# Performance work log

Hardware: AMD Instinct MI355X
Metric: run time of the kernel (lower is better)

The kernel has to match this reference:

```python
import jax, jax.numpy as jnp
import numpy as np

VOCAB, EMB, HID = 100000, 300, 600
B, S, N = 256, 64, 64
MAX_LEVEL = 3  # depth of the fixed 4-ary tree


def _tree():
    parent = np.zeros(N, np.int32)
    level = np.zeros(N, np.int32)
    for i in range(1, N):
        parent[i] = (i - 1) // 4
        level[i] = level[parent[i]] + 1
    return parent, level


def setup_inputs() -> dict:
    key = jax.random.key(0)
    ks = jax.random.split(key, 16)
    parent, level = _tree()
    E_tab = jax.random.normal(ks[0], (VOCAB, EMB), jnp.float32) * 0.1
    E_tab = E_tab.at[0].set(0.0)  # padding_idx=0
    return dict(
        premise_x=jax.random.randint(ks[1], (B, S), 0, VOCAB),
        hypothesis_x=jax.random.randint(ks[2], (B, S), 0, VOCAB),
        p_word_idx=jax.random.randint(ks[3], (B, N), -1, S),  # -1 => ones vector
        p_rel_id=jax.random.randint(ks[4], (B, N), -1, 4),    # 0..2 transformed, -1/3 identity
        h_word_idx=jax.random.randint(ks[5], (B, N), -1, S),
        h_rel_id=jax.random.randint(ks[6], (B, N), -1, 4),
        parent=jnp.asarray(parent),
        level=jnp.asarray(level),
        E_tab=E_tab,
        W_enc=jax.random.normal(ks[7], (3, EMB, EMB), jnp.float32) * 0.1,
        W0_w=jax.random.normal(ks[8], (HID, 6 * EMB), jnp.float32) * 0.1,
        W0_b=jax.random.normal(ks[9], (HID,), jnp.float32) * 0.1,
        W1_w=jax.random.normal(ks[10], (HID, HID), jnp.float32) * 0.1,
        W1_b=jax.random.normal(ks[11], (HID,), jnp.float32) * 0.1,
        W2_w=jax.random.normal(ks[12], (HID, HID), jnp.float32) * 0.1,
        W2_b=jax.random.normal(ks[13], (HID,), jnp.float32) * 0.1,
        Wout_w=jax.random.normal(ks[14], (3, HID), jnp.float32) * 0.1,
        Wout_b=jax.random.normal(ks[15], (3,), jnp.float32) * 0.1,
    )


def _encode_sg(seq, word_idx, rel_id, parent, level, W_enc):
    # Level-synchronous bottom-up evaluation of: leaf -> word,
    # internal -> relu(word * mean(rel-transformed children)).
    Bn, Nn = word_idx.shape
    Ed = seq.shape[-1]
    idx = jnp.clip(word_idx, 0, None)
    word = jnp.take_along_axis(seq, idx[:, :, None], axis=1)        # [B,N,E]
    word = jnp.where((word_idx == -1)[..., None], 1.0, word)        # word_idx==-1 => ones
    h = word
    pflat = (parent[None, :] + (jnp.arange(Bn) * Nn)[:, None]).reshape(-1)
    for l in range(MAX_LEVEL, 0, -1):
        is_child = jnp.broadcast_to(level[None, :] == l, (Bn, Nn))
        # per-relation linear W_enc[r]: h @ W.T (torch Linear, no bias)
        t_all = jnp.einsum('bne,rfe->bnrf', h, W_enc)               # [B,N,3,E]
        sel = jnp.clip(rel_id, 0, 2)[:, :, None, None]
        t = jnp.take_along_axis(t_all, sel, axis=2)[:, :, 0, :]
        t = jnp.where(((rel_id >= 0) & (rel_id <= 2))[..., None], t, h)
        contrib = jnp.where(is_child[..., None], t, 0.0).reshape(Bn * Nn, Ed)
        sums = jnp.zeros((Bn * Nn, Ed), h.dtype).at[pflat].add(contrib)
        counts = jnp.zeros((Bn * Nn,), h.dtype).at[pflat].add(
            is_child.astype(h.dtype).reshape(-1))
        mean = (sums / jnp.maximum(counts, 1.0)[:, None]).reshape(Bn, Nn, Ed)
        has_child = (counts.reshape(Bn, Nn) > 0)
        h = jnp.where(has_child[..., None], jax.nn.relu(word * mean), h)
    return h[:, 0, :]  # root representation


def reference(premise_x, hypothesis_x, p_word_idx, p_rel_id, h_word_idx, h_rel_id,
              parent, level, E_tab, W_enc, W0_w, W0_b, W1_w, W1_b, W2_w, W2_b,
              Wout_w, Wout_b):
    emb_p = E_tab[premise_x]      # [B,S,E]
    emb_h = E_tab[hypothesis_x]
    p_rep = emb_p.sum(axis=1)
    h_rep = emb_h.sum(axis=1)
    p_sg = _encode_sg(emb_p, p_word_idx, p_rel_id, parent, level, W_enc)
    h_sg = _encode_sg(emb_h, h_word_idx, h_rel_id, parent, level, W_enc)
    x = jnp.concatenate([p_rep, h_rep, p_rep - h_rep, p_rep * h_rep,
                         p_sg - h_sg, p_sg * h_sg], axis=1)  # [B,6E]
    h1 = jax.nn.relu(x @ W0_w.T + W0_b)
    h2 = jax.nn.relu(h1 @ W1_w.T + W1_b)
    h3 = jax.nn.relu(h2 @ W2_w.T + W2_b)
    return h3 @ Wout_w.T + Wout_b  # [B,3]
```

## Files before the change

### kernel.cpp

```cpp
#include <hip/hip_runtime.h>

constexpr int NB = 256;
constexpr int NS = 64;
constexpr int NN = 64;
constexpr int NE = 300;
constexpr int NH = 600;

typedef __attribute__((ext_vector_type(8))) short bf16x8;
typedef __attribute__((ext_vector_type(4))) float f32x4;

constexpr int KT0 = 57;
constexpr int KT1 = 19;
constexpr int NJT = 40;
constexpr int HP  = 640;

constexpr size_t OFF_REP = 0;
constexpr size_t SZ_REP  = (size_t)2*NB*NE;
constexpr size_t OFF_ROOT= OFF_REP + SZ_REP;
constexpr size_t OFF_WBF = OFF_ROOT + SZ_REP;
constexpr size_t SZ_WBF  = (size_t)3*20*10*64*8/2;
constexpr size_t OFF_W0S = OFF_WBF + SZ_WBF;
constexpr size_t SZ_W0S  = (size_t)KT0*NJT*64*8/2;
constexpr size_t OFF_W1S = OFF_W0S + SZ_W0S;
constexpr size_t SZ_W1S  = (size_t)KT1*NJT*64*8/2;
constexpr size_t OFF_W2S = OFF_W1S + SZ_W1S;
constexpr size_t OFF_XSW = OFF_W2S + SZ_W1S;
constexpr size_t SZ_XSW  = (size_t)KT0*16*64*8/2;
constexpr size_t OFF_H1  = OFF_XSW + SZ_XSW;
constexpr size_t SZ_H    = (size_t)NB*HP/2;
constexpr size_t OFF_H2  = OFF_H1 + SZ_H;
constexpr size_t OFF_H3  = OFF_H2 + SZ_H;

__device__ __forceinline__ ushort f2bf(float x) {
  unsigned u = __float_as_uint(x);
  unsigned r = (u + 0x7FFFu + ((u >> 16) & 1u)) >> 16;
  return (ushort)r;
}
__device__ __forceinline__ float bf2f(ushort u) {
  return __uint_as_float(((unsigned)u) << 16);
}

constexpr int NSWZ = 3*20*10*64;
constexpr int N0S  = KT0*NJT*64;
constexpr int N1S  = KT1*NJT*64;
constexpr int SETUP_ITEMS  = NSWZ + N0S + 2*N1S;
constexpr int SETUP_BLOCKS = SETUP_ITEMS/256;

__global__ __launch_bounds__(256)
void k_setup(const float* __restrict__ Wenc, const float* __restrict__ W0,
             const float* __restrict__ W1, const float* __restrict__ W2,
             ushort* __restrict__ Wbf, ushort* __restrict__ W0S,
             ushort* __restrict__ W1S, ushort* __restrict__ W2S) {
  int t = blockIdx.x*256 + threadIdx.x;
  if (t < NSWZ) {
    int lane = t & 63, rest = t >> 6;
    int ksi = rest % 10, rnt = rest / 10, nt = rnt % 20, r = rnt / 20;
    int f = nt*16 + (lane & 15), e0 = ksi*32 + (lane >> 4)*8;
    ushort v[8];
    #pragma unroll
    for (int j = 0; j < 8; j++) {
      int e = e0 + j;
      v[j] = (f < NE && e < NE) ? f2bf(Wenc[((size_t)r*NE + f)*NE + e]) : (ushort)0;
    }
    *reinterpret_cast<int4*>(&Wbf[(size_t)t*8]) = *reinterpret_cast<const int4*>(v);
    return;
  }
  t -= NSWZ;
  const float* W; ushort* D; int K;
  if (t < N0S)              { W = W0; D = W0S; K = 6*NE; }
  else { t -= N0S;
    if (t < N1S)            { W = W1; D = W1S; K = NH; }
    else { t -= N1S;          W = W2; D = W2S; K = NH; } }
  int lane = t & 63, g = t >> 6;
  int jt = g % NJT, kt = g / NJT;
  int j  = jt*16 + (lane & 15);
  int kb = kt*32 + (lane >> 4)*8;
  ushort v[8];
  #pragma unroll
  for (int i = 0; i < 8; i++) {
    int k = kb + i;
    v[i] = (j < NH && k < K) ? f2bf(W[(size_t)j*K + k]) : (ushort)0;
  }
  *reinterpret_cast<int4*>(&D[(size_t)t*8]) = *reinterpret_cast<const int4*>(v);
}

constexpr int TS = 328;

__global__ __launch_bounds__(512, 4)
void k_tree(const int* __restrict__ px, const int* __restrict__ hx,
            const int* __restrict__ pwi, const int* __restrict__ prel,
            const int* __restrict__ hwi, const int* __restrict__ hrel,
            const float* __restrict__ Etab, const ushort* __restrict__ Wbf,
            float* __restrict__ rep, float* __restrict__ root) {
  __shared__ __align__(16) ushort hS[64*TS];
  __shared__ __align__(16) float repP[8][304];
  __shared__ int xsh[64];
  __shared__ int wish[64];
  __shared__ int relsh[64];
  const int sb = blockIdx.x;
  const int s = sb >> 8, b = sb & 255;
  const int tid = threadIdx.x;
  const int wave = tid >> 6, lane = tid & 63;

  if (tid < 64) xsh[tid] = ((s ? hx : px) + b*NS)[tid];
  else if (tid < 128) wish[tid-64] = ((s ? hwi : pwi) + b*NN)[tid-64];
  else if (tid < 192) relsh[tid-128] = ((s ? hrel : prel) + b*NN)[tid-128];
  __syncthreads();

  {
    f32x4 a0{0.f,0.f,0.f,0.f}, a1{0.f,0.f,0.f,0.f};
    const int c0 = lane, c1 = lane + 64;
    #pragma unroll 8
    for (int jj = 0; jj < 8; jj++) {
      const float* rowp = &Etab[(size_t)xsh[wave*8 + jj]*NE];
      float4 v0 = *reinterpret_cast<const float4*>(&rowp[c0*4]);
      a0[0] += v0.x; a0[1] += v0.y; a0[2] += v0.z; a0[3] += v0.w;
      if (c1 < 75) {
        float4 v1 = *reinterpret_cast<const float4*>(&rowp[c1*4]);
        a1[0] += v1.x; a1[1] += v1.y; a1[2] += v1.z; a1[3] += v1.w;
      }
    }
    *reinterpret_cast<f32x4*>(&repP[wave][c0*4]) = a0;
    if (c1 < 75) *reinterpret_cast<f32x4*>(&repP[wave][c1*4]) = a1;
  }
  for (int flat = tid; flat < 64*75; flat += 512) {
    int n = flat / 75, c = flat % 75;
    int w = wish[n];
    float4 v;
    if (w < 0) v = float4{1.f,1.f,1.f,1.f};
    else v = *reinterpret_cast<const float4*>(&Etab[(size_t)xsh[w]*NE + c*4]);
    ushort4 o; o.x = f2bf(v.x); o.y = f2bf(v.y); o.z = f2bf(v.z); o.w = f2bf(v.w);
    *reinterpret_cast<ushort4*>(&hS[n*TS + c*4]) = o;
  }
  for (int z = tid; z < 64*10; z += 512) {
    int row = z / 10, cc = z % 10;
    *reinterpret_cast<unsigned*>(&hS[row*TS + 300 + cc*2]) = 0u;
  }
  __syncthreads();

  if (tid < NE) {
    float ssum = 0.f;
    #pragma unroll
    for (int w = 0; w < 8; w++) ssum += repP[w][tid];
    rep[(size_t)sb*NE + tid] = ssum;
  }

  const int mrow = lane & 15, quad = lane >> 4;

  {
    const int mb0 = 21, mb1 = 37, mb2 = 53;
    bf16x8 af[3][10];
    #pragma unroll
    for (int ks = 0; ks < 10; ks++) {
      af[0][ks] = *reinterpret_cast<const bf16x8*>(&hS[(mb0+mrow)*TS + ks*32 + quad*8]);
      af[1][ks] = *reinterpret_cast<const bf16x8*>(&hS[(mb1+mrow)*TS + ks*32 + quad*8]);
      int r2 = min(mb2+mrow, 63);
      af[2][ks] = *reinterpret_cast<const bf16x8*>(&hS[r2*TS + ks*32 + quad*8]);
    }
    __syncthreads();
    for (int pr = wave; pr < 57; pr += 8) {
      int r = pr / 19, nt = pr % 19;
      const ushort* Wb = &Wbf[(size_t)((r*20 + nt)*10)*64*8];
      f32x4 acc0 = f32x4{0.f,0.f,0.f,0.f};
      f32x4 acc1 = f32x4{0.f,0.f,0.f,0.f};
      f32x4 acc2 = f32x4{0.f,0.f,0.f,0.f};
      #pragma unroll
      for (int ks = 0; ks < 10; ks++) {
        bf16x8 bf = *reinterpret_cast<const bf16x8*>(&Wb[((size_t)ks*64 + lane)*8]);
        acc0 = __builtin_amdgcn_mfma_f32_16x16x32_bf16(af[0][ks], bf, acc0, 0, 0, 0);
        acc1 = __builtin_amdgcn_mfma_f32_16x16x32_bf16(af[1][ks], bf, acc1, 0, 0, 0);
        acc2 = __builtin_amdgcn_mfma_f32_16x16x32_bf16(af[2][ks], bf, acc2, 0, 0, 0);
      }
      int f = nt*16 + mrow;
      if (f < NE) {
        #pragma unroll
        for (int reg = 0; reg < 4; reg++) {
          int m = quad*4 + reg;
          int c0 = mb0 + m, c1 = mb1 + m, c2 = mb2 + m;
          if (relsh[c0] == r) hS[c0*TS + f] = f2bf(acc0[reg]);
          if (relsh[c1] == r) hS[c1*TS + f] = f2bf(acc1[reg]);
          if (c2 < 64 && relsh[c2] == r) hS[c2*TS + f] = f2bf(acc2[reg]);
        }
      }
    }
    __syncthreads();
    for (int f = tid; f < NE; f += 512) {
      #pragma unroll
      for (int p = 5; p <= 15; p++) {
        int nc = (p == 15) ? 3 : 4;
        float sum = 0.f;
        for (int j = 0; j < nc; j++) sum += bf2f(hS[(4*p+1+j)*TS + f]);
        float v = bf2f(hS[p*TS + f]) * sum * (1.0f/(float)nc);
        hS[p*TS + f] = f2bf(v > 0.f ? v : 0.f);
      }
    }
    __syncthreads();
  }
  {
    bf16x8 af[10];
    #pragma unroll
    for (int ks = 0; ks < 10; ks++)
      af[ks] = *reinterpret_cast<const bf16x8*>(&hS[(5+mrow)*TS + ks*32 + quad*8]);
    __syncthreads();
    for (int pr = wave; pr < 57; pr += 8) {
      int r = pr / 19, nt = pr % 19;
      const ushort* Wb = &Wbf[(size_t)((r*20 + nt)*10)*64*8];
      f32x4 acc = f32x4{0.f,0.f,0.f,0.f};
      #pragma unroll
      for (int ks = 0; ks < 10; ks++) {
        bf16x8 bf = *reinterpret_cast<const bf16x8*>(&Wb[((size_t)ks*64 + lane)*8]);
        acc = __builtin_amdgcn_mfma_f32_16x16x32_bf16(af[ks], bf, acc, 0, 0, 0);
      }
      int f = nt*16 + mrow;
      if (f < NE) {
        #pragma unroll
        for (int reg = 0; reg < 4; reg++) {
          int c = 5 + quad*4 + reg;
          if (relsh[c] == r) hS[c*TS + f] = f2bf(acc[reg]);
        }
      }
    }
    __syncthreads();
    for (int f = tid; f < NE; f += 512) {
      #pragma unroll
      for (int p = 1; p <= 4; p++) {
        float sum = 0.f;
        #pragma unroll
        for (int j = 0; j < 4; j++) sum += bf2f(hS[(4*p+1+j)*TS + f]);
        float v = bf2f(hS[p*TS + f]) * sum * 0.25f;
        hS[p*TS + f] = f2bf(v > 0.f ? v : 0.f);
      }
    }
    __syncthreads();
  }
  {
    bool rp0 = (relsh[1]==0)|(relsh[2]==0)|(relsh[3]==0)|(relsh[4]==0);
    bool rp1 = (relsh[1]==1)|(relsh[2]==1)|(relsh[3]==1)|(relsh[4]==1);
    bool rp2 = (relsh[1]==2)|(relsh[2]==2)|(relsh[3]==2)|(relsh[4]==2);
    bf16x8 af[10];
    #pragma unroll
    for (int ks = 0; ks < 10; ks++)
      af[ks] = *reinterpret_cast<const bf16x8*>(&hS[(1+min(mrow,3))*TS + ks*32 + quad*8]);
    __syncthreads();
    for (int pr = wave; pr < 57; pr += 8) {
      int r = pr / 19, nt = pr % 19;
      if ((r==0 && !rp0) || (r==1 && !rp1) || (r==2 && !rp2)) continue;
      const ushort* Wb = &Wbf[(size_t)((r*20 + nt)*10)*64*8];
      f32x4 acc = f32x4{0.f,0.f,0.f,0.f};
      #pragma unroll
      for (int ks = 0; ks < 10; ks++) {
        bf16x8 bf = *reinterpret_cast<const bf16x8*>(&Wb[((size_t)ks*64 + lane)*8]);
        acc = __builtin_amdgcn_mfma_f32_16x16x32_bf16(af[ks], bf, acc, 0, 0, 0);
      }
      int f = nt*16 + mrow;
      if (f < NE) {
        #pragma unroll
        for (int reg = 0; reg < 4; reg++) {
          int m = quad*4 + reg;
          if (m < 4 && relsh[1+m] == r) hS[(1+m)*TS + f] = f2bf(acc[reg]);
        }
      }
    }
    __syncthreads();
    for (int f = tid; f < NE; f += 512) {
      float sum = 0.f;
      #pragma unroll
      for (int c = 1; c <= 4; c++) sum += bf2f(hS[c*TS + f]);
      float v = bf2f(hS[0*TS + f]) * sum * 0.25f;
      root[(size_t)sb*NE + f] = v > 0.f ? v : 0.f;
    }
  }
}

constexpr int FEAT_ITEMS  = KT0*16*64;
constexpr int FEAT_BLOCKS = FEAT_ITEMS/256;

__global__ __launch_bounds__(256)
void k_feat(const float* __restrict__ rep, const float* __restrict__ root,
            ushort* __restrict__ Xsw) {
  int t = blockIdx.x*256 + threadIdx.x;
  int lane = t & 63, g = t >> 6;
  int mt = g % 16, kt = g / 16;
  int b  = mt*16 + (lane & 15);
  int kb = kt*32 + (lane >> 4)*8;
  const float* rp = rep  + (size_t)b*NE;
  const float* rh = rep  + (size_t)(NB+b)*NE;
  const float* tp = root + (size_t)b*NE;
  const float* th = root + (size_t)(NB+b)*NE;
  ushort v[8];
  #pragma unroll
  for (int i = 0; i < 8; i++) {
    int k = kb + i;
    float x = 0.f;
    if (k < 6*NE) {
      int seg = k / NE, e = k - seg*NE;
      switch (seg) {
        case 0:  x = rp[e]; break;
        case 1:  x = rh[e]; break;
        case 2:  x = rp[e] - rh[e]; break;
        case 3:  x = rp[e] * rh[e]; break;
        case 4:  x = tp[e] - th[e]; break;
        default: x = tp[e] * th[e]; break;
      }
    }
    v[i] = f2bf(x);
  }
  *reinterpret_cast<int4*>(&Xsw[(size_t)t*8]) = *reinterpret_cast<const int4*>(v);
}

__global__ __launch_bounds__(256)
void k_fc(const ushort* __restrict__ A, const ushort* __restrict__ Wsw,
          const float* __restrict__ bias, ushort* __restrict__ hout,
          int nkt, int mode) {
  __shared__ __align__(16) float red[4*4*64*4];
  const int tid = threadIdx.x, wv = tid >> 6, lane = tid & 63;
  const int bx = blockIdx.x, by = blockIdx.y;

  f32x4 acc[4];
  #pragma unroll
  for (int q = 0; q < 4; q++) acc[q] = f32x4{0.f,0.f,0.f,0.f};

  for (int kt = wv; kt < nkt; kt += 4) {
    bf16x8 a;
    if (mode == 0)
      a = *reinterpret_cast<const bf16x8*>(&A[(((size_t)kt*16 + bx)*64 + lane)*8]);
    else
      a = *reinterpret_cast<const bf16x8*>(
          &A[(size_t)(bx*16 + (lane & 15))*HP + kt*32 + (lane >> 4)*8]);
    #pragma unroll
    for (int q = 0; q < 4; q++) {
      bf16x8 w = *reinterpret_cast<const bf16x8*>(
          &Wsw[(((size_t)kt*NJT + by*4 + q)*64 + lane)*8]);
      acc[q] = __builtin_amdgcn_mfma_f32_16x16x32_bf16(a, w, acc[q], 0, 0, 0);
    }
  }
  #pragma unroll
  for (int q = 0; q < 4; q++)
    *reinterpret_cast<f32x4*>(&red[(((size_t)q*4 + wv)*64 + lane)*4]) = acc[q];
  __syncthreads();
  f32x4 s{0.f,0.f,0.f,0.f};
  #pragma unroll
  for (int w = 0; w < 4; w++) {
    f32x4 p = *reinterpret_cast<f32x4*>(&red[(((size_t)wv*4 + w)*64 + lane)*4]);
    s[0] += p[0]; s[1] += p[1]; s[2] += p[2]; s[3] += p[3];
  }
  int row0 = bx*16 + (lane >> 4)*4;
  int j = (by*4 + wv)*16 + (lane & 15);
  if (j < 608) {
    float bj = (j < NH) ? bias[j] : 0.f;
    #pragma unroll
    for (int r = 0; r < 4; r++) {
      float v = s[r] + bj;
      v = v > 0.f ? v : 0.f;
      hout[(size_t)(row0 + r)*HP + j] = (j < NH) ? f2bf(v) : (ushort)0;
    }
  }
}

__global__ __launch_bounds__(64)
void k_out(const ushort* __restrict__ h3, const float* __restrict__ Wout,
           const float* __restrict__ bout, float* __restrict__ out) {
  int b = blockIdx.x, tid = threadIdx.x;
  float a0 = 0.f, a1 = 0.f, a2 = 0.f;
  for (int k = tid; k < NH; k += 64) {
    float xv = bf2f(h3[(size_t)b*HP + k]);
    a0 += xv * Wout[k];
    a1 += xv * Wout[NH + k];
    a2 += xv * Wout[2*NH + k];
  }
  #pragma unroll
  for (int off = 32; off > 0; off >>= 1) {
    a0 += __shfl_down(a0, off, 64);
    a1 += __shfl_down(a1, off, 64);
    a2 += __shfl_down(a2, off, 64);
  }
  if (tid == 0) {
    out[b*3 + 0] = a0 + bout[0];
    out[b*3 + 1] = a1 + bout[1];
    out[b*3 + 2] = a2 + bout[2];
  }
}

extern "C" void kernel_launch(void* const* d_in, const int* in_sizes, int n_in,
                              void* d_out, int out_size, void* d_ws, size_t ws_size,
                              hipStream_t stream) {
  const int*   px    = (const int*)d_in[0];
  const int*   hx    = (const int*)d_in[1];
  const int*   pwi   = (const int*)d_in[2];
  const int*   prel  = (const int*)d_in[3];
  const int*   hwi   = (const int*)d_in[4];
  const int*   hrel  = (const int*)d_in[5];
  const float* Etab  = (const float*)d_in[8];
  const float* Wenc  = (const float*)d_in[9];
  const float* W0w   = (const float*)d_in[10];
  const float* W0b   = (const float*)d_in[11];
  const float* W1w   = (const float*)d_in[12];
  const float* W1b   = (const float*)d_in[13];
  const float* W2w   = (const float*)d_in[14];
  const float* W2b   = (const float*)d_in[15];
  const float* Woutw = (const float*)d_in[16];
  const float* Woutb = (const float*)d_in[17];

  float* ws   = (float*)d_ws;
  float*  rep  = ws + OFF_REP;
  float*  root = ws + OFF_ROOT;
  ushort* Wbf  = (ushort*)(ws + OFF_WBF);
  ushort* W0S  = (ushort*)(ws + OFF_W0S);
  ushort* W1S  = (ushort*)(ws + OFF_W1S);
  ushort* W2S  = (ushort*)(ws + OFF_W2S);
  ushort* Xsw  = (ushort*)(ws + OFF_XSW);
  ushort* h1   = (ushort*)(ws + OFF_H1);
  ushort* h2   = (ushort*)(ws + OFF_H2);
  ushort* h3   = (ushort*)(ws + OFF_H3);
  float* outp = (float*)d_out;

  k_setup<<<dim3(SETUP_BLOCKS), dim3(256), 0, stream>>>(
      Wenc, W0w, W1w, W2w, Wbf, W0S, W1S, W2S);
  k_tree<<<dim3(2*NB), dim3(512), 0, stream>>>(
      px, hx, pwi, prel, hwi, hrel, Etab, Wbf, rep, root);
  k_feat<<<dim3(FEAT_BLOCKS), dim3(256), 0, stream>>>(rep, root, Xsw);
  k_fc<<<dim3(16,10), dim3(256), 0, stream>>>(Xsw, W0S, W0b, h1, KT0, 0);
  k_fc<<<dim3(16,10), dim3(256), 0, stream>>>(h1,  W1S, W1b, h2, KT1, 1);
  k_fc<<<dim3(16,10), dim3(256), 0, stream>>>(h2,  W2S, W2b, h3, KT1, 1);
  k_out<<<dim3(NB), dim3(64), 0, stream>>>(h3, Woutw, Woutb, outp);
}
```

Measured before the change: 301.7 us.

## Write transformed children to separate LDS buffer and drop register-cached A fragments

Relation-transformed child rows now go to a separate LDS buffer tS, so the MFMA loops can read A operands straight from LDS instead of caching up to 30 bf16x8 fragments in registers and syncing before overwriting hS. The launch-bound occupancy hint is removed. The embedding-sum work and the word-gather work are also split between wave groups so they run concurrently. The cost is more LDS (about 28 KB extra) and more LDS reads inside the MFMA loops, which may lower the number of resident blocks.

Result: slower. 310.9 us (+3.0%).

```diff
diff --git a/kernel.cpp b/kernel.cpp
--- a/kernel.cpp
+++ b/kernel.cpp
@@ -85,15 +85,17 @@
 }
 
 constexpr int TS = 328;
-
-__global__ __launch_bounds__(512, 4)
+constexpr int TR = 44;
+
+__global__ __launch_bounds__(512)
 void k_tree(const int* __restrict__ px, const int* __restrict__ hx,
             const int* __restrict__ pwi, const int* __restrict__ prel,
             const int* __restrict__ hwi, const int* __restrict__ hrel,
             const float* __restrict__ Etab, const ushort* __restrict__ Wbf,
             float* __restrict__ rep, float* __restrict__ root) {
   __shared__ __align__(16) ushort hS[64*TS];
-  __shared__ __align__(16) float repP[8][304];
+  __shared__ __align__(16) ushort tS[TR*TS];
+  __shared__ __align__(16) float repP[4][304];
   __shared__ int xsh[64];
   __shared__ int wish[64];
   __shared__ int relsh[64];
@@ -107,12 +109,12 @@
   else if (tid < 192) relsh[tid-128] = ((s ? hrel : prel) + b*NN)[tid-128];
   __syncthreads();
 
-  {
+  if (wave < 4) {
     f32x4 a0{0.f,0.f,0.f,0.f}, a1{0.f,0.f,0.f,0.f};
     const int c0 = lane, c1 = lane + 64;
     #pragma unroll 8
-    for (int jj = 0; jj < 8; jj++) {
-      const float* rowp = &Etab[(size_t)xsh[wave*8 + jj]*NE];
+    for (int jj = 0; jj < 16; jj++) {
+      const float* rowp = &Etab[(size_t)xsh[wave*16 + jj]*NE];
       float4 v0 = *reinterpret_cast<const float4*>(&rowp[c0*4]);
       a0[0] += v0.x; a0[1] += v0.y; a0[2] += v0.z; a0[3] += v0.w;
       if (c1 < 75) {
@@ -122,42 +124,34 @@
     }
     *reinterpret_cast<f32x4*>(&repP[wave][c0*4]) = a0;
     if (c1 < 75) *reinterpret_cast<f32x4*>(&repP[wave][c1*4]) = a1;
-  }
-  for (int flat = tid; flat < 64*75; flat += 512) {
-    int n = flat / 75, c = flat % 75;
-    int w = wish[n];
-    float4 v;
-    if (w < 0) v = float4{1.f,1.f,1.f,1.f};
-    else v = *reinterpret_cast<const float4*>(&Etab[(size_t)xsh[w]*NE + c*4]);
-    ushort4 o; o.x = f2bf(v.x); o.y = f2bf(v.y); o.z = f2bf(v.z); o.w = f2bf(v.w);
-    *reinterpret_cast<ushort4*>(&hS[n*TS + c*4]) = o;
-  }
-  for (int z = tid; z < 64*10; z += 512) {
-    int row = z / 10, cc = z % 10;
-    *reinterpret_cast<unsigned*>(&hS[row*TS + 300 + cc*2]) = 0u;
+    for (int z = tid; z < 64*10; z += 256) {
+      int row = z / 10, cc = z % 10;
+      *reinterpret_cast<unsigned*>(&hS[row*TS + 300 + cc*2]) = 0u;
+    }
+  } else {
+    for (int flat = tid - 256; flat < 64*75; flat += 256) {
+      int n = flat / 75, c = flat % 75;
+      int w = wish[n];
+      float4 v;
+      if (w < 0) v = float4{1.f,1.f,1.f,1.f};
+      else v = *reinterpret_cast<const float4*>(&Etab[(size_t)xsh[w]*NE + c*4]);
+      ushort4 o; o.x = f2bf(v.x); o.y = f2bf(v.y); o.z = f2bf(v.z); o.w = f2bf(v.w);
+      *reinterpret_cast<ushort4*>(&hS[n*TS + c*4]) = o;
+    }
   }
   __syncthreads();
 
   if (tid < NE) {
-    float ssum = 0.f;
-    #pragma unroll
-    for (int w = 0; w < 8; w++) ssum += repP[w][tid];
+    float ssum = repP[0][tid] + repP[1][tid] + repP[2][tid] + repP[3][tid];
     rep[(size_t)sb*NE + tid] = ssum;
   }
 
   const int mrow = lane & 15, quad = lane >> 4;
 
   {
-    const int mb0 = 21, mb1 = 37, mb2 = 53;
-    bf16x8 af[3][10];
-    #pragma unroll
-    for (int ks = 0; ks < 10; ks++) {
-      af[0][ks] = *reinterpret_cast<const bf16x8*>(&hS[(mb0+mrow)*TS + ks*32 + quad*8]);
-      af[1][ks] = *reinterpret_cast<const bf16x8*>(&hS[(mb1+mrow)*TS + ks*32 + quad*8]);
-      int r2 = min(mb2+mrow, 63);
-      af[2][ks] = *reinterpret_cast<const bf16x8*>(&hS[r2*TS + ks*32 + quad*8]);
-    }
-    __syncthreads();
+    const int ra0 = (21 + mrow)*TS;
+    const int ra1 = (37 + mrow)*TS;
+    const int ra2 = min(53 + mrow, 63)*TS;
     for (int pr = wave; pr < 57; pr += 8) {
       int r = pr / 19, nt = pr % 19;
       const ushort* Wb = &Wbf[(size_t)((r*20 + nt)*10)*64*8];
@@ -167,19 +161,22 @@
       #pragma unroll
       for (int ks = 0; ks < 10; ks++) {
         bf16x8 bf = *reinterpret_cast<const bf16x8*>(&Wb[((size_t)ks*64 + lane)*8]);
-        acc0 = __builtin_amdgcn_mfma_f32_16x16x32_bf16(af[0][ks], bf, acc0, 0, 0, 0);
-        acc1 = __builtin_amdgcn_mfma_f32_16x16x32_bf16(af[1][ks], bf, acc1, 0, 0, 0);
-        acc2 = __builtin_amdgcn_mfma_f32_16x16x32_bf16(af[2][ks], bf, acc2, 0, 0, 0);
+        bf16x8 a0 = *reinterpret_cast<const bf16x8*>(&hS[ra0 + ks*32 + quad*8]);
+        bf16x8 a1 = *reinterpret_cast<const bf16x8*>(&hS[ra1 + ks*32 + quad*8]);
+        bf16x8 a2 = *reinterpret_cast<const bf16x8*>(&hS[ra2 + ks*32 + quad*8]);
+        acc0 = __builtin_amdgcn_mfma_f32_16x16x32_bf16(a0, bf, acc0, 0, 0, 0);
+        acc1 = __builtin_amdgcn_mfma_f32_16x16x32_bf16(a1, bf, acc1, 0, 0, 0);
+        acc2 = __builtin_amdgcn_mfma_f32_16x16x32_bf16(a2, bf, acc2, 0, 0, 0);
       }
       int f = nt*16 + mrow;
       if (f < NE) {
         #pragma unroll
         for (int reg = 0; reg < 4; reg++) {
           int m = quad*4 + reg;
-          int c0 = mb0 + m, c1 = mb1 + m, c2 = mb2 + m;
-          if (relsh[c0] == r) hS[c0*TS + f] = f2bf(acc0[reg]);
-          if (relsh[c1] == r) hS[c1*TS + f] = f2bf(acc1[reg]);
-          if (c2 < 64 && relsh[c2] == r) hS[c2*TS + f] = f2bf(acc2[reg]);
+          int c0 = 21 + m, c1 = 37 + m, c2 = 53 + m;
+          if (relsh[c0] == r) tS[(c0-20)*TS + f] = f2bf(acc0[reg]);
+          if (relsh[c1] == r) tS[(c1-20)*TS + f] = f2bf(acc1[reg]);
+          if (c2 < 64 && relsh[c2] == r) tS[(c2-20)*TS + f] = f2bf(acc2[reg]);
         }
       }
     }
@@ -189,7 +186,11 @@
       for (int p = 5; p <= 15; p++) {
         int nc = (p == 15) ? 3 : 4;
         float sum = 0.f;
-        for (int j = 0; j < nc; j++) sum += bf2f(hS[(4*p+1+j)*TS + f]);
+        for (int j = 0; j < nc; j++) {
+          int c = 4*p + 1 + j, rl = relsh[c];
+          ushort hv = (rl >= 0 && rl <= 2) ? tS[(c-20)*TS + f] : hS[c*TS + f];
+          sum += bf2f(hv);
+        }
         float v = bf2f(hS[p*TS + f]) * sum * (1.0f/(float)nc);
         hS[p*TS + f] = f2bf(v > 0.f ? v : 0.f);
       }
@@ -197,11 +198,7 @@
     __syncthreads();
   }
   {
-    bf16x8 af[10];
-    #pragma unroll
-    for (int ks = 0; ks < 10; ks++)
-      af[ks] = *reinterpret_cast<const bf16x8*>(&hS[(5+mrow)*TS + ks*32 + quad*8]);
-    __syncthreads();
+    const int ra = (5 + mrow)*TS;
     for (int pr = wave; pr < 57; pr += 8) {
       int r = pr / 19, nt = pr % 19;
       const ushort* Wb = &Wbf[(size_t)((r*20 + nt)*10)*64*8];
@@ -209,14 +206,15 @@
       #pragma unroll
       for (int ks = 0; ks < 10; ks++) {
         bf16x8 bf = *reinterpret_cast<const bf16x8*>(&Wb[((size_t)ks*64 + lane)*8]);
-        acc = __builtin_amdgcn_mfma_f32_16x16x32_bf16(af[ks], bf, acc, 0, 0, 0);
+        bf16x8 a  = *reinterpret_cast<const bf16x8*>(&hS[ra + ks*32 + quad*8]);
+        acc = __builtin_amdgcn_mfma_f32_16x16x32_bf16(a, bf, acc, 0, 0, 0);
       }
       int f = nt*16 + mrow;
       if (f < NE) {
         #pragma unroll
         for (int reg = 0; reg < 4; reg++) {
           int c = 5 + quad*4 + reg;
-          if (relsh[c] == r) hS[c*TS + f] = f2bf(acc[reg]);
+          if (relsh[c] == r) tS[(c-5)*TS + f] = f2bf(acc[reg]);
         }
       }
     }
@@ -226,7 +224,11 @@
       for (int p = 1; p <= 4; p++) {
         float sum = 0.f;
         #pragma unroll
-        for (int j = 0; j < 4; j++) sum += bf2f(hS[(4*p+1+j)*TS + f]);
+        for (int j = 0; j < 4; j++) {
+          int c = 4*p + 1 + j, rl = relsh[c];
+          ushort hv = (rl >= 0 && rl <= 2) ? tS[(c-5)*TS + f] : hS[c*TS + f];
+          sum += bf2f(hv);
+        }
         float v = bf2f(hS[p*TS + f]) * sum * 0.25f;
         hS[p*TS + f] = f2bf(v > 0.f ? v : 0.f);
       }
@@ -237,11 +239,7 @@
     bool rp0 = (relsh[1]==0)|(relsh[2]==0)|(relsh[3]==0)|(relsh[4]==0);
     bool rp1 = (relsh[1]==1)|(relsh[2]==1)|(relsh[3]==1)|(relsh[4]==1);
     bool rp2 = (relsh[1]==2)|(relsh[2]==2)|(relsh[3]==2)|(relsh[4]==2);
-    bf16x8 af[10];
-    #pragma unroll
-    for (int ks = 0; ks < 10; ks++)
-      af[ks] = *reinterpret_cast<const bf16x8*>(&hS[(1+min(mrow,3))*TS + ks*32 + quad*8]);
-    __syncthreads();
+    const int ra = (1 + min(mrow, 3))*TS;
     for (int pr = wave; pr < 57; pr += 8) {
       int r = pr / 19, nt = pr % 19;
       if ((r==0 && !rp0) || (r==1 && !rp1) || (r==2 && !rp2)) continue;
@@ -250,14 +248,15 @@
       #pragma unroll
       for (int ks = 0; ks < 10; ks++) {
         bf16x8 bf = *reinterpret_cast<const bf16x8*>(&Wb[((size_t)ks*64 + lane)*8]);
-        acc = __builtin_amdgcn_mfma_f32_16x16x32_bf16(af[ks], bf, acc, 0, 0, 0);
+        bf16x8 a  = *reinterpret_cast<const bf16x8*>(&hS[ra + ks*32 + quad*8]);
+        acc = __builtin_amdgcn_mfma_f32_16x16x32_bf16(a, bf, acc, 0, 0, 0);
       }
       int f = nt*16 + mrow;
       if (f < NE) {
         #pragma unroll
         for (int reg = 0; reg < 4; reg++) {
           int m = quad*4 + reg;
-          if (m < 4 && relsh[1+m] == r) hS[(1+m)*TS + f] = f2bf(acc[reg]);
+          if (m < 4 && relsh[1+m] == r) tS[m*TS + f] = f2bf(acc[reg]);
         }
       }
     }
@@ -265,7 +264,11 @@
     for (int f = tid; f < NE; f += 512) {
       float sum = 0.f;
       #pragma unroll
-      for (int c = 1; c <= 4; c++) sum += bf2f(hS[c*TS + f]);
+      for (int c = 1; c <= 4; c++) {
+        int rl = relsh[c];
+        ushort hv = (rl >= 0 && rl <= 2) ? tS[(c-1)*TS + f] : hS[c*TS + f];
+        sum += bf2f(hv);
+      }
       float v = bf2f(hS[0*TS + f]) * sum * 0.25f;
       root[(size_t)sb*NE + f] = v > 0.f ? v : 0.f;
     }
```
